# Kernel tuning notes

Measured on AMD Instinct MI355X. Metric: run time of the kernel, lower is better.

## Reference

```python
import math
import jax, jax.numpy as jnp
import numpy as np

L = 4        # number of base-MLP layers
B = 16       # batch of weight-space samples
N = 256      # base-MLP width (n_in = n_out = N)
C_IN = 16    # input channels per weight entry
C_OUT = 16   # output channels per weight entry
HID = 64     # siren hidden dim
W0 = 1.0
W0_FIRST = 30.0
FINAL_NORM = math.sqrt((2 * L + 7) * C_IN)


def setup_inputs() -> dict:
    key = jax.random.key(0)
    ks = jax.random.split(key, 17)
    d = {}
    for i in range(L):
        d[f"w{i}"] = jax.random.normal(ks[i], (B, N, N, C_IN), jnp.float32) * 0.02
        d[f"b{i}"] = jax.random.normal(ks[L + i], (B, N, C_IN), jnp.float32) * 0.02
    def u(k, shape, scale):
        return jax.random.uniform(k, shape, jnp.float32, -scale, scale)
    # SIREN-style init scales
    d["s_w0"] = u(ks[8], (3, HID), 1.0 / 3.0)
    d["s_b0"] = u(ks[9], (HID,), 1.0 / math.sqrt(3.0))
    d["s_w1"] = u(ks[10], (HID, HID), math.sqrt(6.0 / HID) / W0)
    d["s_b1"] = u(ks[11], (HID,), 1.0 / math.sqrt(HID))
    d["s_w2"] = u(ks[12], (HID, HID), math.sqrt(6.0 / HID) / W0)
    d["s_b2"] = u(ks[13], (HID,), 1.0 / math.sqrt(HID))
    d["s_wo"] = u(ks[14], (HID, C_IN * C_OUT), math.sqrt(6.0 / HID) / W0)
    d["s_bo"] = u(ks[15], (C_IN * C_OUT,), 1.0 / math.sqrt(HID))
    return d


def _siren(x, sp):
    sw0, sb0, sw1, sb1, sw2, sb2, swo, sbo = sp
    h = jnp.sin(W0_FIRST * (x @ sw0 + sb0))
    h = jnp.sin(W0 * (h @ sw1 + sb1))
    h = jnp.sin(W0 * (h @ sw2 + sb2))
    return (h @ swo + sbo) / FINAL_NORM


def _forward(ws, bs, sp):
    term_idx = jnp.linspace(-1.0, 1.0, num=14)
    layer_idx = jnp.linspace(-1.0, 1.0, num=L)
    grid = jnp.stack(jnp.meshgrid(layer_idx, layer_idx, indexing='ij'), axis=-1)  # (L,L,2)

    g_in = jnp.concatenate([jnp.broadcast_to(grid, (4, L, L, 2)),
                            jnp.broadcast_to(term_idx[:4, None, None, None], (4, L, L, 1))], -1)
    global_terms = _siren(g_in, sp).reshape(4, L, L, C_IN, C_OUT)

    dgrid = jnp.transpose(jnp.diagonal(grid))          # (L,2)
    d_in = jnp.concatenate([jnp.broadcast_to(dgrid, (6, L, 2)),
                            jnp.broadcast_to(term_idx[4:10, None, None], (6, L, 1))], -1)
    diag_terms = _siren(d_in, sp).reshape(6, L, C_IN, C_OUT)

    p1 = jnp.transpose(jnp.diagonal(grid, offset=1))   # (L-1,2)
    p1_in = jnp.concatenate([jnp.broadcast_to(p1, (2, L - 1, 2)),
                             jnp.broadcast_to(term_idx[10:12, None, None], (2, L - 1, 1))], -1)
    diag_p1 = _siren(p1_in, sp).reshape(2, L - 1, C_IN, C_OUT)

    m1 = jnp.transpose(jnp.diagonal(grid, offset=-1))  # (L-1,2)
    m1_in = jnp.concatenate([jnp.broadcast_to(m1, (2, L - 1, 2)),
                             jnp.broadcast_to(term_idx[12:14, None, None], (2, L - 1, 1))], -1)
    diag_m1 = _siren(m1_in, sp).reshape(2, L - 1, C_IN, C_OUT)

    t_w_otherw, t_w_otherb = global_terms[0], global_terms[1]
    t_b_otherw, t_b_otherb = global_terms[2], global_terms[3]
    t_w_wrow, t_w_wcol, t_w_w = diag_terms[0], diag_terms[1], diag_terms[2]
    t_w_b, t_b_wcol, t_bb = diag_terms[3], diag_terms[4], diag_terms[5]
    t_w_wm1, t_w_bm1 = diag_m1[0], diag_m1[1]
    t_w_wp1, t_b_wp1 = diag_p1[0], diag_p1[1]

    rsums = [jnp.mean(w, axis=1) for w in ws]          # (B,K,c)
    csums = [jnp.mean(w, axis=2) for w in ws]          # (B,J,c)
    allsums = jnp.stack([jnp.mean(r, axis=1) for r in rsums], -1)  # (B,c,L)
    sums_b = jnp.stack([jnp.mean(b, axis=1) for b in bs], -1)      # (B,c,L)

    outs = []
    for i in range(L):
        ow = jnp.einsum('bjkc,cd->bjkd', ws[i], t_w_w[i])
        ow += jnp.einsum('bcl,lcd->bd', allsums, t_w_otherw[i])[:, None, None, :]
        ow += jnp.einsum('bcl,lcd->bd', sums_b, t_w_otherb[i])[:, None, None, :]
        ow += jnp.einsum('bjc,cd->bjd', csums[i], t_w_wcol[i])[:, :, None, :]
        ow += jnp.einsum('bkc,cd->bkd', rsums[i], t_w_wrow[i])[:, None, :, :]
        ow += jnp.einsum('bkc,cd->bkd', bs[i], t_w_b[i])[:, None, :, :]
        if i > 0:
            ow += jnp.einsum('bjc,cd->bjd', rsums[i - 1], t_w_wm1[i - 1])[:, :, None, :]
            ow += jnp.einsum('bjc,cd->bjd', bs[i - 1], t_w_bm1[i - 1])[:, :, None, :]
        if i < L - 1:
            ow += jnp.einsum('bkc,cd->bkd', csums[i + 1], t_w_wp1[i])[:, None, :, :]
        ob = jnp.einsum('bjc,cd->bjd', bs[i], t_bb[i])
        ob += jnp.einsum('bkc,cd->bkd', rsums[i], t_b_wcol[i])
        if i < L - 1:
            ob += jnp.einsum('bkc,cd->bkd', csums[i + 1], t_b_wp1[i])
        ob += jnp.einsum('bcl,lcd->bd', allsums, t_b_otherw[i])[:, None, :]
        ob += jnp.einsum('bcl,lcd->bd', sums_b, t_b_otherb[i])[:, None, :]
        outs += [ow, ob]
    return tuple(outs)


def reference(w0, w1, w2, w3, b0, b1, b2, b3,
              s_w0, s_b0, s_w1, s_b1, s_w2, s_b2, s_wo, s_bo):
    return _forward([w0, w1, w2, w3], [b0, b1, b2, b3],
                    (s_w0, s_b0, s_w1, s_b1, s_w2, s_b2, s_wo, s_bo))
```

## Files before the change

kernel.cpp:

```cpp
#include <hip/hip_runtime.h>
#include <math.h>

#define DEV_INLINE __device__ __forceinline__

constexpr int Nn = 256;
constexpr size_t SZW = (size_t)16 * 256 * 256 * 16;
constexpr size_t SZB = (size_t)16 * 256 * 16;
constexpr size_t OSTRIDE = SZW + SZB;

constexpr int T_GT  = 0;
constexpr int T_DT  = 16384;
constexpr int T_P1  = 22528;
constexpr int T_M1  = 24064;
constexpr int O_RSF = 25600;
constexpr int O_CS  = 287744;
constexpr int O_AS  = 549888;
constexpr int O_BS  = 550912;
constexpr int O_AROW= 551936;
constexpr int O_BCOL= 814080;
constexpr int O_RSP = 1076224;

DEV_INLINE void f4acc(float4& a, const float4 b) { a.x += b.x; a.y += b.y; a.z += b.z; a.w += b.w; }
DEV_INLINE float4 f4add(const float4 a, const float4 b) { return make_float4(a.x + b.x, a.y + b.y, a.z + b.z, a.w + b.w); }
DEV_INLINE void f4fma(float4& a, float s, const float4 t) {
    a.x = fmaf(s, t.x, a.x); a.y = fmaf(s, t.y, a.y);
    a.z = fmaf(s, t.z, a.z); a.w = fmaf(s, t.w, a.w);
}
DEV_INLINE void f4shfl_xor_acc(float4& a, int m) {
    a.x += __shfl_xor(a.x, m); a.y += __shfl_xor(a.y, m);
    a.z += __shfl_xor(a.z, m); a.w += __shfl_xor(a.w, m);
}

__global__ __launch_bounds__(64) void siren_kernel(
    const float* __restrict__ sw0, const float* __restrict__ sb0,
    const float* __restrict__ sw1, const float* __restrict__ sb1,
    const float* __restrict__ sw2, const float* __restrict__ sb2,
    const float* __restrict__ swo, const float* __restrict__ sbo,
    float* __restrict__ ws) {
    __shared__ float h[64];
    const int p = blockIdx.x, t = threadIdx.x;
    const float lv[4] = {-1.f, -1.f / 3.f, 1.f / 3.f, 1.f};
    float x, y, tt;
    if (p < 64)      { int tm = p >> 4, a = (p >> 2) & 3, bb = p & 3; x = lv[a];   y = lv[bb];  tt = -1.f + 2.f * tm / 13.f; }
    else if (p < 88) { int q = p - 64; int tm = q >> 2, a = q & 3;    x = lv[a];   y = lv[a];   tt = -1.f + 2.f * (4 + tm) / 13.f; }
    else if (p < 94) { int q = p - 88; int tm = q / 3, a = q % 3;     x = lv[a];   y = lv[a+1]; tt = -1.f + 2.f * (10 + tm) / 13.f; }
    else             { int q = p - 94; int tm = q / 3, a = q % 3;     x = lv[a+1]; y = lv[a];   tt = -1.f + 2.f * (12 + tm) / 13.f; }
    float v = sinf(30.f * (x * sw0[t] + y * sw0[64 + t] + tt * sw0[128 + t] + sb0[t]));
    h[t] = v; __syncthreads();
    float v1 = sb1[t];
    for (int u = 0; u < 64; ++u) v1 += h[u] * sw1[u * 64 + t];
    v1 = sinf(v1);
    __syncthreads(); h[t] = v1; __syncthreads();
    float v2 = sb2[t];
    for (int u = 0; u < 64; ++u) v2 += h[u] * sw2[u * 64 + t];
    v2 = sinf(v2);
    __syncthreads(); h[t] = v2; __syncthreads();
    const float inv_fn = 0.06454972243679028f;
    for (int m = 0; m < 4; ++m) {
        int o = m * 64 + t;
        float vo = sbo[o];
        for (int u = 0; u < 64; ++u) vo += h[u] * swo[u * 256 + o];
        ws[p * 256 + o] = vo * inv_fn;
    }
}

__global__ __launch_bounds__(64) void reduce_b_kernel(
    const float4* __restrict__ b0, const float4* __restrict__ b1,
    const float4* __restrict__ b2, const float4* __restrict__ b3,
    float* __restrict__ ws) {
    const int z = blockIdx.x;
    const int l = z >> 4, b = z & 15;
    const float4* bp = ((l == 0) ? b0 : (l == 1) ? b1 : (l == 2) ? b2 : b3) + (size_t)b * Nn * 4;
    const int lane = threadIdx.x;
    const int c4 = lane & 3, part = lane >> 2;
    float4 acc = make_float4(0.f, 0.f, 0.f, 0.f);
    for (int s = 0; s < 16; ++s) f4acc(acc, bp[(size_t)(part + s * 16) * 4 + c4]);
#pragma unroll
    for (int m = 4; m < 64; m <<= 1) f4shfl_xor_acc(acc, m);
    if (lane < 4) {
        float* dst = ws + O_BS + (size_t)z * 16 + lane * 4;
        dst[0] = acc.x; dst[1] = acc.y; dst[2] = acc.z; dst[3] = acc.w;
    }
}

__global__ __launch_bounds__(256) void reduce_w_kernel(
    const float4* __restrict__ w0, const float4* __restrict__ w1,
    const float4* __restrict__ w2, const float4* __restrict__ w3,
    float* __restrict__ ws, int bbase) {
    const int strip = blockIdx.x;
    const int lbg = blockIdx.y;
    const int l = lbg >> 3, b = bbase + (lbg & 7);
    const float4* __restrict__ w = (l == 0) ? w0 : (l == 1) ? w1 : (l == 2) ? w2 : w3;
    const int tid = threadIdx.x;
    const int wv = tid >> 6, lane = tid & 63;
    const int plb = l * 16 + b;

    __shared__ float4 csbuf[8][4][4];
    __shared__ float4 abuf[4][4];

    float4 racc0 = make_float4(0, 0, 0, 0), racc1 = racc0, racc2 = racc0, racc3 = racc0;
    const size_t rowb = ((size_t)(b * Nn + strip * 8)) * 1024;

#pragma unroll
    for (int r = 0; r < 8; ++r) {
        const float4* wp = w + rowb + (size_t)r * 1024 + tid;
        float4 v0 = wp[0], v1 = wp[256], v2 = wp[512], v3 = wp[768];
        f4acc(racc0, v0); f4acc(racc1, v1); f4acc(racc2, v2); f4acc(racc3, v3);
        float4 s = f4add(f4add(v0, v1), f4add(v2, v3));
        f4shfl_xor_acc(s, 4); f4shfl_xor_acc(s, 8);
        f4shfl_xor_acc(s, 16); f4shfl_xor_acc(s, 32);
        if (lane < 4) csbuf[r][wv][lane] = s;
    }
    __syncthreads();

    if (tid < 32) {
        const int r = tid >> 2, cc = tid & 3;
        float4 cv = f4add(f4add(csbuf[r][0][cc], csbuf[r][1][cc]),
                          f4add(csbuf[r][2][cc], csbuf[r][3][cc]));
        ((float4*)(ws + O_CS))[(size_t)(plb * Nn + strip * 8 + r) * 4 + cc] = cv;
    }

    float4* part = (float4*)(ws + O_RSP) + (size_t)(plb * 32 + strip) * 1024;
    part[tid]       = racc0;
    part[256 + tid] = racc1;
    part[512 + tid] = racc2;
    part[768 + tid] = racc3;

    float4 a = f4add(f4add(racc0, racc1), f4add(racc2, racc3));
    f4shfl_xor_acc(a, 4); f4shfl_xor_acc(a, 8);
    f4shfl_xor_acc(a, 16); f4shfl_xor_acc(a, 32);
    if (lane < 4) abuf[wv][lane] = a;
    __syncthreads();
    if (tid < 4) {
        float4 av = f4add(f4add(abuf[0][tid], abuf[1][tid]), f4add(abuf[2][tid], abuf[3][tid]));
        float* dst = ws + O_AS + (size_t)plb * 16 + tid * 4;
        atomicAdd(dst + 0, av.x); atomicAdd(dst + 1, av.y);
        atomicAdd(dst + 2, av.z); atomicAdd(dst + 3, av.w);
    }
}

__global__ __launch_bounds__(256) void fold_rs_kernel(float* __restrict__ ws, int bbase) {
    const int g = blockIdx.x * 256 + threadIdx.x;
    const int rest = g & 1023, lbg = g >> 10;
    const int l = lbg >> 3, b = bbase + (lbg & 7);
    const int plb = l * 16 + b;
    const float4* part = (const float4*)(ws + O_RSP) + (size_t)(plb * 32) * 1024 + rest;
    float4 acc = part[0];
#pragma unroll
    for (int s = 1; s < 32; ++s) f4acc(acc, part[(size_t)s * 1024]);
    ((float4*)(ws + O_RSF))[(size_t)plb * 1024 + rest] = acc;
}

__global__ __launch_bounds__(256) void vectors_kernel(
    const float* __restrict__ bias0, const float* __restrict__ bias1,
    const float* __restrict__ bias2, const float* __restrict__ bias3,
    float* __restrict__ ws, float* __restrict__ out, int bbase) {
    const int g = blockIdx.x * 256 + threadIdx.x;
    const int d = g & 15, n = (g >> 4) & 255, bg = (g >> 12) & 7, l = g >> 15;
    const int b = bbase + bg;
    const float invN = 1.f / 256.f, invNN = 1.f / 65536.f;
    const float* bias[4] = {bias0, bias1, bias2, bias3};
    const size_t rowi = (size_t)((l * 16 + b) * 256 + n) * 16;
    const float* cs = ws + O_CS + rowi;
    const float* rs = ws + O_RSF + rowi;
    const float* bv = bias[l] + (size_t)(b * 256 + n) * 16;
    const float* dt = ws + T_DT;
    const float* Twrow  = dt + (0 * 4 + l) * 256;
    const float* Twcol  = dt + (1 * 4 + l) * 256;
    const float* Twb    = dt + (3 * 4 + l) * 256;
    const float* Tbwcol = dt + (4 * 4 + l) * 256;
    const float* Tbb    = dt + (5 * 4 + l) * 256;
    float arow = 0.f, bcol = 0.f, ob = 0.f;
#pragma unroll
    for (int c = 0; c < 16; ++c) {
        float cm = cs[c] * invN, rm = rs[c] * invN, bb = bv[c];
        arow += cm * Twcol[c * 16 + d];
        bcol += rm * Twrow[c * 16 + d] + bb * Twb[c * 16 + d];
        ob   += rm * Tbwcol[c * 16 + d] + bb * Tbb[c * 16 + d];
    }
    if (l > 0) {
        const float* rsm = ws + O_RSF + (size_t)(((l - 1) * 16 + b) * 256 + n) * 16;
        const float* bvm = bias[l - 1] + (size_t)(b * 256 + n) * 16;
        const float* Twm1 = ws + T_M1 + (l - 1) * 256;
        const float* Tbm1 = ws + T_M1 + (3 + l - 1) * 256;
#pragma unroll
        for (int c = 0; c < 16; ++c)
            arow += rsm[c] * invN * Twm1[c * 16 + d] + bvm[c] * Tbm1[c * 16 + d];
    }
    if (l < 3) {
        const float* csp = ws + O_CS + (size_t)(((l + 1) * 16 + b) * 256 + n) * 16;
        const float* Twp1  = ws + T_P1 + l * 256;
        const float* Tbwp1 = ws + T_P1 + (3 + l) * 256;
#pragma unroll
        for (int c = 0; c < 16; ++c) {
            float cp = csp[c] * invN;
            bcol += cp * Twp1[c * 16 + d];
            ob   += cp * Tbwp1[c * 16 + d];
        }
    }
#pragma unroll
    for (int ll = 0; ll < 4; ++ll) {
        const float* as_ = ws + O_AS + (size_t)(ll * 16 + b) * 16;
        const float* bs_ = ws + O_BS + (size_t)(ll * 16 + b) * 16;
        const float* g0 = ws + ((0 * 4 + l) * 4 + ll) * 256;
        const float* g1 = ws + ((1 * 4 + l) * 4 + ll) * 256;
        const float* g2 = ws + ((2 * 4 + l) * 4 + ll) * 256;
        const float* g3 = ws + ((3 * 4 + l) * 4 + ll) * 256;
#pragma unroll
        for (int c = 0; c < 16; ++c) {
            float am = as_[c] * invNN, bm = bs_[c] * invN;
            arow += am * g0[c * 16 + d] + bm * g1[c * 16 + d];
            ob   += am * g2[c * 16 + d] + bm * g3[c * 16 + d];
        }
    }
    ws[O_AROW + rowi + d] = arow;
    ws[O_BCOL + rowi + d] = bcol;
    out[(size_t)l * OSTRIDE + SZW + (size_t)(b * 256 + n) * 16 + d] = ob;
}

__global__ __launch_bounds__(256) void transform_kernel(
    const float4* __restrict__ w0, const float4* __restrict__ w1,
    const float4* __restrict__ w2, const float4* __restrict__ w3,
    const float* __restrict__ ws, float4* __restrict__ out, int bbase) {
    const int j = blockIdx.x, bg = blockIdx.y, l = blockIdx.z;
    const int b = bbase + bg;
    const float4* __restrict__ w = (l == 0) ? w0 : (l == 1) ? w1 : (l == 2) ? w2 : w3;
    const int tid = threadIdx.x;
    const int d4 = tid & 3, kk = tid >> 2;
    const float4* T4 = (const float4*)ws + (T_DT / 4) + (2 * 4 + l) * 64;
    float4 t[16];
#pragma unroll
    for (int c = 0; c < 16; ++c) t[c] = T4[c * 4 + d4];
    const size_t rowbase = (size_t)(b * 256 + j) * 256;
    const float4* Ar = (const float4*)(ws + O_AROW);
    const float4* Bc = (const float4*)(ws + O_BCOL) + (size_t)(l * 16 + b) * 256 * 4 + d4;
    const float4 arow = Ar[(size_t)((l * 16 + b) * 256 + j) * 4 + d4];
    const size_t outb = (size_t)l * (OSTRIDE / 4) + rowbase * 4 + d4;
#pragma unroll
    for (int s = 0; s < 4; ++s) {
        const int k = s * 64 + kk;
        float4 acc = f4add(arow, Bc[(size_t)k * 4]);
        const float4* wp = w + (rowbase + k) * 4;
        float4 v0 = wp[0], v1 = wp[1], v2 = wp[2], v3 = wp[3];
        f4fma(acc, v0.x, t[0]);  f4fma(acc, v0.y, t[1]);  f4fma(acc, v0.z, t[2]);  f4fma(acc, v0.w, t[3]);
        f4fma(acc, v1.x, t[4]);  f4fma(acc, v1.y, t[5]);  f4fma(acc, v1.z, t[6]);  f4fma(acc, v1.w, t[7]);
        f4fma(acc, v2.x, t[8]);  f4fma(acc, v2.y, t[9]);  f4fma(acc, v2.z, t[10]); f4fma(acc, v2.w, t[11]);
        f4fma(acc, v3.x, t[12]); f4fma(acc, v3.y, t[13]); f4fma(acc, v3.z, t[14]); f4fma(acc, v3.w, t[15]);
        out[outb + (size_t)k * 4] = acc;
    }
}

extern "C" void kernel_launch(void* const* d_in, const int* in_sizes, int n_in,
                              void* d_out, int out_size, void* d_ws, size_t ws_size,
                              hipStream_t stream) {
    const float *W[4], *Bv[4], *S[8];
    if (in_sizes[1] == in_sizes[0]) {
        for (int i = 0; i < 4; ++i) { W[i] = (const float*)d_in[i]; Bv[i] = (const float*)d_in[4 + i]; }
    } else {
        for (int i = 0; i < 4; ++i) { W[i] = (const float*)d_in[2 * i]; Bv[i] = (const float*)d_in[2 * i + 1]; }
    }
    for (int k = 0; k < 8; ++k) S[k] = (const float*)d_in[8 + k];
    float* ws = (float*)d_ws;
    float* out = (float*)d_out;

    hipMemsetAsync(ws + O_AS, 0, 1024 * sizeof(float), stream);
    siren_kernel<<<100, 64, 0, stream>>>(S[0], S[1], S[2], S[3], S[4], S[5], S[6], S[7], ws);
    reduce_b_kernel<<<64, 64, 0, stream>>>((const float4*)Bv[0], (const float4*)Bv[1],
                                           (const float4*)Bv[2], (const float4*)Bv[3], ws);
    for (int g = 0; g < 2; ++g) {
        const int bbase = 8 * g;
        reduce_w_kernel<<<dim3(32, 32), 256, 0, stream>>>(
            (const float4*)W[0], (const float4*)W[1], (const float4*)W[2], (const float4*)W[3], ws, bbase);
        fold_rs_kernel<<<128, 256, 0, stream>>>(ws, bbase);
        vectors_kernel<<<512, 256, 0, stream>>>(Bv[0], Bv[1], Bv[2], Bv[3], ws, out, bbase);
        transform_kernel<<<dim3(256, 8, 4), 256, 0, stream>>>(
            (const float4*)W[0], (const float4*)W[1], (const float4*)W[2], (const float4*)W[3],
            ws, (float4*)out, bbase);
    }
}
```

Measured before the change: 625.9 us.

## Process all batches in one pass and fuse siren with bias reduction

Merges the bias-sum reduction into the siren kernel as extra blocks, which saves one launch. It also drops the two-half batch loop, so each of reduce_w, fold, vectors and transform now runs once over all 16 batches. The reduce_w strips grow from 8 to 16 rows, which halves the partial row-sum buffers that fold has to combine. The aim is fewer launches and more parallel work per launch. The risk is losing the cache reuse that the half-batch chunking gave: the weight tensors read by transform would no longer fit in the last-level cache after reduce_w.

```diff
diff --git a/kernel.cpp b/kernel.cpp
--- a/kernel.cpp
+++ b/kernel.cpp
@@ -31,14 +31,33 @@
     a.z += __shfl_xor(a.z, m); a.w += __shfl_xor(a.w, m);
 }
 
-__global__ __launch_bounds__(64) void siren_kernel(
+__global__ __launch_bounds__(64) void siren_b_kernel(
     const float* __restrict__ sw0, const float* __restrict__ sb0,
     const float* __restrict__ sw1, const float* __restrict__ sb1,
     const float* __restrict__ sw2, const float* __restrict__ sb2,
     const float* __restrict__ swo, const float* __restrict__ sbo,
+    const float4* __restrict__ b0, const float4* __restrict__ b1,
+    const float4* __restrict__ b2, const float4* __restrict__ b3,
     float* __restrict__ ws) {
+    const int blk = blockIdx.x;
+    if (blk >= 100) {
+        const int z = blk - 100;
+        const int l = z >> 4, b = z & 15;
+        const float4* bp = ((l == 0) ? b0 : (l == 1) ? b1 : (l == 2) ? b2 : b3) + (size_t)b * Nn * 4;
+        const int lane = threadIdx.x;
+        const int c4 = lane & 3, part = lane >> 2;
+        float4 acc = make_float4(0.f, 0.f, 0.f, 0.f);
+        for (int s = 0; s < 16; ++s) f4acc(acc, bp[(size_t)(part + s * 16) * 4 + c4]);
+#pragma unroll
+        for (int m = 4; m < 64; m <<= 1) f4shfl_xor_acc(acc, m);
+        if (lane < 4) {
+            float* dst = ws + O_BS + (size_t)z * 16 + lane * 4;
+            dst[0] = acc.x; dst[1] = acc.y; dst[2] = acc.z; dst[3] = acc.w;
+        }
+        return;
+    }
     __shared__ float h[64];
-    const int p = blockIdx.x, t = threadIdx.x;
+    const int p = blk, t = threadIdx.x;
     const float lv[4] = {-1.f, -1.f / 3.f, 1.f / 3.f, 1.f};
     float x, y, tt;
     if (p < 64)      { int tm = p >> 4, a = (p >> 2) & 3, bb = p & 3; x = lv[a];   y = lv[bb];  tt = -1.f + 2.f * tm / 13.f; }
@@ -64,45 +83,25 @@
     }
 }
 
-__global__ __launch_bounds__(64) void reduce_b_kernel(
-    const float4* __restrict__ b0, const float4* __restrict__ b1,
-    const float4* __restrict__ b2, const float4* __restrict__ b3,
-    float* __restrict__ ws) {
-    const int z = blockIdx.x;
-    const int l = z >> 4, b = z & 15;
-    const float4* bp = ((l == 0) ? b0 : (l == 1) ? b1 : (l == 2) ? b2 : b3) + (size_t)b * Nn * 4;
-    const int lane = threadIdx.x;
-    const int c4 = lane & 3, part = lane >> 2;
-    float4 acc = make_float4(0.f, 0.f, 0.f, 0.f);
-    for (int s = 0; s < 16; ++s) f4acc(acc, bp[(size_t)(part + s * 16) * 4 + c4]);
-#pragma unroll
-    for (int m = 4; m < 64; m <<= 1) f4shfl_xor_acc(acc, m);
-    if (lane < 4) {
-        float* dst = ws + O_BS + (size_t)z * 16 + lane * 4;
-        dst[0] = acc.x; dst[1] = acc.y; dst[2] = acc.z; dst[3] = acc.w;
-    }
-}
-
 __global__ __launch_bounds__(256) void reduce_w_kernel(
     const float4* __restrict__ w0, const float4* __restrict__ w1,
     const float4* __restrict__ w2, const float4* __restrict__ w3,
-    float* __restrict__ ws, int bbase) {
+    float* __restrict__ ws) {
     const int strip = blockIdx.x;
-    const int lbg = blockIdx.y;
-    const int l = lbg >> 3, b = bbase + (lbg & 7);
+    const int plb = blockIdx.y;
+    const int l = plb >> 4, b = plb & 15;
     const float4* __restrict__ w = (l == 0) ? w0 : (l == 1) ? w1 : (l == 2) ? w2 : w3;
     const int tid = threadIdx.x;
     const int wv = tid >> 6, lane = tid & 63;
-    const int plb = l * 16 + b;
-
-    __shared__ float4 csbuf[8][4][4];
+
+    __shared__ float4 csbuf[16][4][4];
     __shared__ float4 abuf[4][4];
 
     float4 racc0 = make_float4(0, 0, 0, 0), racc1 = racc0, racc2 = racc0, racc3 = racc0;
-    const size_t rowb = ((size_t)(b * Nn + strip * 8)) * 1024;
-
-#pragma unroll
-    for (int r = 0; r < 8; ++r) {
+    const size_t rowb = ((size_t)(b * Nn + strip * 16)) * 1024;
+
+#pragma unroll
+    for (int r = 0; r < 16; ++r) {
         const float4* wp = w + rowb + (size_t)r * 1024 + tid;
         float4 v0 = wp[0], v1 = wp[256], v2 = wp[512], v3 = wp[768];
         f4acc(racc0, v0); f4acc(racc1, v1); f4acc(racc2, v2); f4acc(racc3, v3);
@@ -113,14 +112,14 @@
     }
     __syncthreads();
 
-    if (tid < 32) {
+    if (tid < 64) {
         const int r = tid >> 2, cc = tid & 3;
         float4 cv = f4add(f4add(csbuf[r][0][cc], csbuf[r][1][cc]),
                           f4add(csbuf[r][2][cc], csbuf[r][3][cc]));
-        ((float4*)(ws + O_CS))[(size_t)(plb * Nn + strip * 8 + r) * 4 + cc] = cv;
-    }
-
-    float4* part = (float4*)(ws + O_RSP) + (size_t)(plb * 32 + strip) * 1024;
+        ((float4*)(ws + O_CS))[(size_t)(plb * Nn + strip * 16 + r) * 4 + cc] = cv;
+    }
+
+    float4* part = (float4*)(ws + O_RSP) + (size_t)(plb * 16 + strip) * 1024;
     part[tid]       = racc0;
     part[256 + tid] = racc1;
     part[512 + tid] = racc2;
@@ -139,25 +138,22 @@
     }
 }
 
-__global__ __launch_bounds__(256) void fold_rs_kernel(float* __restrict__ ws, int bbase) {
+__global__ __launch_bounds__(256) void fold_rs_kernel(float* __restrict__ ws) {
     const int g = blockIdx.x * 256 + threadIdx.x;
-    const int rest = g & 1023, lbg = g >> 10;
-    const int l = lbg >> 3, b = bbase + (lbg & 7);
-    const int plb = l * 16 + b;
-    const float4* part = (const float4*)(ws + O_RSP) + (size_t)(plb * 32) * 1024 + rest;
+    const int rest = g & 1023, plb = g >> 10;
+    const float4* part = (const float4*)(ws + O_RSP) + (size_t)(plb * 16) * 1024 + rest;
     float4 acc = part[0];
 #pragma unroll
-    for (int s = 1; s < 32; ++s) f4acc(acc, part[(size_t)s * 1024]);
+    for (int s = 1; s < 16; ++s) f4acc(acc, part[(size_t)s * 1024]);
     ((float4*)(ws + O_RSF))[(size_t)plb * 1024 + rest] = acc;
 }
 
 __global__ __launch_bounds__(256) void vectors_kernel(
     const float* __restrict__ bias0, const float* __restrict__ bias1,
     const float* __restrict__ bias2, const float* __restrict__ bias3,
-    float* __restrict__ ws, float* __restrict__ out, int bbase) {
+    float* __restrict__ ws, float* __restrict__ out) {
     const int g = blockIdx.x * 256 + threadIdx.x;
-    const int d = g & 15, n = (g >> 4) & 255, bg = (g >> 12) & 7, l = g >> 15;
-    const int b = bbase + bg;
+    const int d = g & 15, n = (g >> 4) & 255, b = (g >> 12) & 15, l = g >> 16;
     const float invN = 1.f / 256.f, invNN = 1.f / 65536.f;
     const float* bias[4] = {bias0, bias1, bias2, bias3};
     const size_t rowi = (size_t)((l * 16 + b) * 256 + n) * 16;
@@ -221,9 +217,8 @@
 __global__ __launch_bounds__(256) void transform_kernel(
     const float4* __restrict__ w0, const float4* __restrict__ w1,
     const float4* __restrict__ w2, const float4* __restrict__ w3,
-    const float* __restrict__ ws, float4* __restrict__ out, int bbase) {
-    const int j = blockIdx.x, bg = blockIdx.y, l = blockIdx.z;
-    const int b = bbase + bg;
+    const float* __restrict__ ws, float4* __restrict__ out) {
+    const int j = blockIdx.x, b = blockIdx.y, l = blockIdx.z;
     const float4* __restrict__ w = (l == 0) ? w0 : (l == 1) ? w1 : (l == 2) ? w2 : w3;
     const int tid = threadIdx.x;
     const int d4 = tid & 3, kk = tid >> 2;
@@ -264,17 +259,14 @@
     float* out = (float*)d_out;
 
     hipMemsetAsync(ws + O_AS, 0, 1024 * sizeof(float), stream);
-    siren_kernel<<<100, 64, 0, stream>>>(S[0], S[1], S[2], S[3], S[4], S[5], S[6], S[7], ws);
-    reduce_b_kernel<<<64, 64, 0, stream>>>((const float4*)Bv[0], (const float4*)Bv[1],
+    siren_b_kernel<<<164, 64, 0, stream>>>(S[0], S[1], S[2], S[3], S[4], S[5], S[6], S[7],
+                                           (const float4*)Bv[0], (const float4*)Bv[1],
                                            (const float4*)Bv[2], (const float4*)Bv[3], ws);
-    for (int g = 0; g < 2; ++g) {
-        const int bbase = 8 * g;
-        reduce_w_kernel<<<dim3(32, 32), 256, 0, stream>>>(
-            (const float4*)W[0], (const float4*)W[1], (const float4*)W[2], (const float4*)W[3], ws, bbase);
-        fold_rs_kernel<<<128, 256, 0, stream>>>(ws, bbase);
-        vectors_kernel<<<512, 256, 0, stream>>>(Bv[0], Bv[1], Bv[2], Bv[3], ws, out, bbase);
-        transform_kernel<<<dim3(256, 8, 4), 256, 0, stream>>>(
-            (const float4*)W[0], (const float4*)W[1], (const float4*)W[2], (const float4*)W[3],
-            ws, (float4*)out, bbase);
-    }
-}
+    reduce_w_kernel<<<dim3(16, 64), 256, 0, stream>>>(
+        (const float4*)W[0], (const float4*)W[1], (const float4*)W[2], (const float4*)W[3], ws);
+    fold_rs_kernel<<<256, 256, 0, stream>>>(ws);
+    vectors_kernel<<<1024, 256, 0, stream>>>(Bv[0], Bv[1], Bv[2], Bv[3], ws, out);
+    transform_kernel<<<dim3(256, 16, 4), 256, 0, stream>>>(
+        (const float4*)W[0], (const float4*)W[1], (const float4*)W[2], (const float4*)W[3],
+        ws, (float4*)out);
+}
```

New measurement: 640.2 us. 1.02x slower.
